# Kernel optimization log

Hardware: AMD Instinct MI355X
Metric: run time of the kernel (lower is better)

Reference implementation:

```python
import jax, jax.numpy as jnp
import numpy as np

STATE_DIM = 2
HIDDEN = 1024
N_SKILLS = 5
N_ACTIONS = 4
BATCH = 65536


def setup_inputs() -> dict:
    key = jax.random.key(0)
    ks = jax.random.split(key, 8)
    def lin_init(k, fan_in, shape):
        bound = 1.0 / np.sqrt(fan_in)
        return jax.random.uniform(k, shape, jnp.float32, -bound, bound)
    return {
        "s": jax.random.normal(ks[0], (BATCH, STATE_DIM), jnp.float32),
        "skill_idx": jax.random.randint(ks[1], (BATCH,), 0, N_SKILLS, jnp.int32),
        "W1": lin_init(ks[2], STATE_DIM, (STATE_DIM, HIDDEN)),
        "b1": lin_init(ks[3], STATE_DIM, (HIDDEN,)),
        "W2": lin_init(ks[4], HIDDEN, (HIDDEN, HIDDEN)),
        "b2": lin_init(ks[5], HIDDEN, (HIDDEN,)),
        "W_heads": lin_init(ks[6], HIDDEN, (N_SKILLS, HIDDEN, N_ACTIONS)),
        "b_heads": lin_init(ks[7], HIDDEN, (N_SKILLS, N_ACTIONS)),
    }


def reference(s, skill_idx, W1, b1, W2, b2, W_heads, b_heads):
    # shared feature MLP: Linear -> ReLU -> Linear -> ReLU
    h = jax.nn.relu(s @ W1 + b1)            # [B, H]
    feat = jax.nn.relu(h @ W2 + b2)         # [B, H]
    # per-sample skill head: gather weights then one batched contraction
    Wg = W_heads[skill_idx]                 # [B, H, A]
    bg = b_heads[skill_idx]                 # [B, A]
    return jnp.einsum('bh,bha->ba', feat, Wg) + bg  # [B, A]
```

## Files before the change

### kernel.cpp

```cpp
#include <hip/hip_runtime.h>

typedef __bf16 bf16x8 __attribute__((ext_vector_type(8)));
typedef __bf16 bf16x4 __attribute__((ext_vector_type(4)));
typedef float  floatx4 __attribute__((ext_vector_type(4)));

#define GLOBAL_AS __attribute__((address_space(1)))
#define LOCAL_AS  __attribute__((address_space(3)))

static constexpr int HID = 1024;
static constexpr int BM  = 256;
static constexpr int BN  = 256;
static constexpr int BK  = 32;
static constexpr int NT  = HID / BK;

__device__ __forceinline__ void h8(bf16x8& d, float s0, float s1,
                                   const float4& w0a, const float4& w0b,
                                   const float4& w1a, const float4& w1b,
                                   const float4& ba,  const float4& bb) {
    d[0] = (__bf16)fmaxf(fmaf(s1, w1a.x, fmaf(s0, w0a.x, ba.x)), 0.f);
    d[1] = (__bf16)fmaxf(fmaf(s1, w1a.y, fmaf(s0, w0a.y, ba.y)), 0.f);
    d[2] = (__bf16)fmaxf(fmaf(s1, w1a.z, fmaf(s0, w0a.z, ba.z)), 0.f);
    d[3] = (__bf16)fmaxf(fmaf(s1, w1a.w, fmaf(s0, w0a.w, ba.w)), 0.f);
    d[4] = (__bf16)fmaxf(fmaf(s1, w1b.x, fmaf(s0, w0b.x, bb.x)), 0.f);
    d[5] = (__bf16)fmaxf(fmaf(s1, w1b.y, fmaf(s0, w0b.y, bb.y)), 0.f);
    d[6] = (__bf16)fmaxf(fmaf(s1, w1b.z, fmaf(s0, w0b.z, bb.z)), 0.f);
    d[7] = (__bf16)fmaxf(fmaf(s1, w1b.w, fmaf(s0, w0b.w, bb.w)), 0.f);
}

__global__ __launch_bounds__(256)
void prep_all(const float* __restrict__ W2, const float* __restrict__ WH,
              __bf16* __restrict__ W2T, __bf16* __restrict__ WHT,
              float* __restrict__ OUT) {
    int b = blockIdx.x;
    if (b < 256) {
        ((float4*)OUT)[(size_t)b * 256 + threadIdx.x]
            = make_float4(0.f, 0.f, 0.f, 0.f);
        return;
    }
    b -= 256;
    if (b < 256) {
        __shared__ __align__(16) __bf16 tile[64][72];
        const int bx = b & 15;
        const int by = b >> 4;
        const int a  = threadIdx.x & 63;
        const int bb = threadIdx.x >> 6;
#pragma unroll
        for (int r = 0; r < 16; ++r) {
            const int k = r * 4 + bb;
            tile[a][k] = (__bf16)W2[(size_t)(by * 64 + k) * HID + bx * 64 + a];
        }
        __syncthreads();
        const int n_loc = threadIdx.x & 63;
        const int w     = threadIdx.x >> 6;
        const int nt    = bx >> 2;
        const int row   = (bx & 3) * 64 + n_loc;
#pragma unroll
        for (int h = 0; h < 2; ++h) {
            const int ko   = w * 2 + h;
            const int kt   = by * 2 + (ko >> 2);
            const int quad = ko & 3;
            const bf16x8 v = *(const bf16x8*)&tile[n_loc][ko * 8];
            const size_t idx = ((size_t)(nt * NT + kt) * 4 + quad) * 256 + row;
            *(bf16x8*)(W2T + idx * 8) = v;
        }
    } else {
        const int r = b - 256;
        const int s = r >> 2, a = r & 3;
        for (int k = threadIdx.x; k < HID; k += 256) {
            const float v = (r < 20) ? WH[((size_t)s * HID + k) * 4 + a] : 0.f;
            WHT[(size_t)(k >> 3) * 256 + r * 8 + (k & 7)] = (__bf16)v;
        }
    }
}

__global__ __launch_bounds__(512, 2)
void policy_main(const float* __restrict__ S,  const int* __restrict__ SK,
                 const float* __restrict__ W1, const float* __restrict__ B1,
                 const __bf16* __restrict__ W2T, const float* __restrict__ B2,
                 const __bf16* __restrict__ WHT, const float* __restrict__ BH,
                 float* __restrict__ OUT) {
    __shared__ __align__(16) char smem[131072];
    __bf16* A0    = (__bf16*)smem;
    __bf16* A1    = (__bf16*)(smem + 16384);
    __bf16* Bb    = (__bf16*)(smem + 32768);
    __bf16* featW = (__bf16*)smem;

    const int tid  = threadIdx.x;
    const int lane = tid & 63;
    const int wv   = tid >> 6;
    const int l15  = lane & 15;
    const int quad = lane >> 4;
    const int wm   = wv >> 2;
    const int wn   = wv & 3;
    const int n8   = blockIdx.x >> 8;
    const int g    = blockIdx.x & 255;
    const size_t i0 = (size_t)g * BM;

    const int octA = wv & 3;
    const int sgrp = wv >> 2;

    floatx4 acc[8][4] = {};

    float2 sv[2];
    sv[0] = *(const float2*)(S + (i0 + sgrp * 64 + lane) * 2);
    sv[1] = *(const float2*)(S + (i0 + 128 + sgrp * 64 + lane) * 2);

    float4 w0a = *(const float4*)(W1 + octA * 8);
    float4 w0b = *(const float4*)(W1 + octA * 8 + 4);
    float4 w1a = *(const float4*)(W1 + HID + octA * 8);
    float4 w1b = *(const float4*)(W1 + HID + octA * 8 + 4);
    float4 bba = *(const float4*)(B1 + octA * 8);
    float4 bbb = *(const float4*)(B1 + octA * 8 + 4);

#pragma unroll
    for (int t = 0; t < 2; ++t)
#pragma unroll
        for (int L = 0; L < 2; ++L) {
            const int c  = wv * 2 + L;
            const int q  = c >> 2;
            const int r0 = (c & 3) * 64;
            const __bf16* gp = W2T
                + ((size_t)((n8 * NT + t) * 4 + q) * 256 + r0 + lane) * 8;
            __builtin_amdgcn_global_load_lds((GLOBAL_AS void*)gp,
                (LOCAL_AS void*)(Bb + t * 8192 + (q * 256 + r0) * 8), 16, 0, 0);
        }

#pragma unroll
    for (int k = 0; k < 2; ++k) {
        const int smp = k * 128 + sgrp * 64 + lane;
        bf16x8 hv;
        h8(hv, sv[k].x, sv[k].y, w0a, w0b, w1a, w1b, bba, bbb);
        *(bf16x8*)(A0 + (octA * 256 + smp) * 8) = hv;
    }
    asm volatile("s_waitcnt vmcnt(2)" ::: "memory");
    asm volatile("s_waitcnt lgkmcnt(0)" ::: "memory");
    __builtin_amdgcn_s_barrier();

    int bcur = 0, bstg = 2;
#pragma unroll 1
    for (int t = 0; t < NT; ++t) {
        __bf16* Ac = (t & 1) ? A1 : A0;
        __bf16* An = (t & 1) ? A0 : A1;
        const __bf16* Bc = Bb + bcur * 8192;

        bf16x8 wf[4], hf[4];
#pragma unroll
        for (int f = 0; f < 4; ++f)
            wf[f] = *(const bf16x8*)(Bc + (quad * 256 + wn * 64 + f * 16 + l15) * 8);
#pragma unroll
        for (int f = 0; f < 4; ++f)
            hf[f] = *(const bf16x8*)(Ac + (quad * 256 + wm * 128 + f * 16 + l15) * 8);
        if (t < NT - 1) {
            const float* wp = W1 + (t + 1) * BK + octA * 8;
            w0a = *(const float4*)(wp);
            w0b = *(const float4*)(wp + 4);
            w1a = *(const float4*)(wp + HID);
            w1b = *(const float4*)(wp + HID + 4);
            bba = *(const float4*)(B1 + (t + 1) * BK + octA * 8);
            bbb = *(const float4*)(B1 + (t + 1) * BK + octA * 8 + 4);
        }
        if (t < NT - 2) {
#pragma unroll
            for (int L = 0; L < 2; ++L) {
                const int c  = wv * 2 + L;
                const int q  = c >> 2;
                const int r0 = (c & 3) * 64;
                const __bf16* gp = W2T
                    + ((size_t)((n8 * NT + (t + 2)) * 4 + q) * 256 + r0 + lane) * 8;
                __builtin_amdgcn_global_load_lds((GLOBAL_AS void*)gp,
                    (LOCAL_AS void*)(Bb + bstg * 8192 + (q * 256 + r0) * 8), 16, 0, 0);
            }
        }
        __builtin_amdgcn_s_barrier();
        asm volatile("s_waitcnt lgkmcnt(0)" ::: "memory");
        __builtin_amdgcn_s_setprio(1);
#pragma unroll
        for (int fm = 0; fm < 4; ++fm)
#pragma unroll
            for (int fn = 0; fn < 4; ++fn)
                acc[fm][fn] = __builtin_amdgcn_mfma_f32_16x16x32_bf16(
                    wf[fn], hf[fm], acc[fm][fn], 0, 0, 0);
        __builtin_amdgcn_s_setprio(0);
        __builtin_amdgcn_s_barrier();

        bf16x8 hf2[4];
#pragma unroll
        for (int f = 0; f < 4; ++f)
            hf2[f] = *(const bf16x8*)(Ac + (quad * 256 + wm * 128 + 64 + f * 16 + l15) * 8);
        if (t < NT - 1) {
#pragma unroll
            for (int k = 0; k < 2; ++k) {
                const int smp = k * 128 + sgrp * 64 + lane;
                bf16x8 hv;
                h8(hv, sv[k].x, sv[k].y, w0a, w0b, w1a, w1b, bba, bbb);
                *(bf16x8*)(An + (octA * 256 + smp) * 8) = hv;
            }
        }
        __builtin_amdgcn_s_barrier();
        asm volatile("s_waitcnt lgkmcnt(0)" ::: "memory");
        __builtin_amdgcn_s_setprio(1);
#pragma unroll
        for (int fm = 0; fm < 4; ++fm)
#pragma unroll
            for (int fn = 0; fn < 4; ++fn)
                acc[fm + 4][fn] = __builtin_amdgcn_mfma_f32_16x16x32_bf16(
                    wf[fn], hf2[fm], acc[fm + 4][fn], 0, 0, 0);
        __builtin_amdgcn_s_setprio(0);
        asm volatile("s_waitcnt vmcnt(2)" ::: "memory");
        __builtin_amdgcn_s_barrier();

        bcur = (bcur == 2) ? 0 : bcur + 1;
        bstg = (bstg == 2) ? 0 : bstg + 1;
    }

#pragma unroll
    for (int fn = 0; fn < 4; ++fn) {
        const int fcb = wn * 64 + fn * 16 + quad * 4;
        const float4 b2v = *(const float4*)(B2 + n8 * 256 + fcb);
        const int o = fcb >> 3, j = fcb & 7;
#pragma unroll
        for (int fm = 0; fm < 8; ++fm) {
            const int smp = wm * 128 + fm * 16 + l15;
            const floatx4 v = acc[fm][fn];
            bf16x4 p;
            p[0] = (__bf16)fmaxf(v[0] + b2v.x, 0.f);
            p[1] = (__bf16)fmaxf(v[1] + b2v.y, 0.f);
            p[2] = (__bf16)fmaxf(v[2] + b2v.z, 0.f);
            p[3] = (__bf16)fmaxf(v[3] + b2v.w, 0.f);
            *(bf16x4*)(featW + (o * 256 + smp) * 8 + j) = p;
        }
    }
    __syncthreads();

    floatx4 hacc[2][2] = {};
#pragma unroll
    for (int f2 = 0; f2 < 2; ++f2) {
        const int row = wv * 32 + f2 * 16 + l15;
#pragma unroll
        for (int ks2 = 0; ks2 < 8; ++ks2) {
            const bf16x8 fa = *(const bf16x8*)(featW
                                 + ((ks2 * 4 + quad) * 256 + row) * 8);
#pragma unroll
            for (int t2 = 0; t2 < 2; ++t2) {
                const int r  = t2 * 16 + l15;
                const int og = n8 * 32 + ks2 * 4 + quad;
                const bf16x8 wb = *(const bf16x8*)(WHT + ((size_t)og * 32 + r) * 8);
                hacc[f2][t2] = __builtin_amdgcn_mfma_f32_16x16x32_bf16(
                    fa, wb, hacc[f2][t2], 0, 0, 0);
            }
        }
    }

#pragma unroll
    for (int f2 = 0; f2 < 2; ++f2)
#pragma unroll
        for (int j = 0; j < 4; ++j) {
            const int smp = wv * 32 + f2 * 16 + quad * 4 + j;
            const int sk  = SK[i0 + smp];
#pragma unroll
            for (int t2 = 0; t2 < 2; ++t2) {
                const int hc = t2 * 16 + l15;
                const int d  = hc - sk * 4;
                if (d >= 0 && d < 4) {
                    float v = hacc[f2][t2][j];
                    if (n8 == 0) v += BH[hc];
                    atomicAdd(&OUT[(i0 + smp) * 4 + d], v);
                }
            }
        }
}

extern "C" void kernel_launch(void* const* d_in, const int* in_sizes, int n_in,
                              void* d_out, int out_size, void* d_ws, size_t ws_size,
                              hipStream_t stream) {
    const float* S  = (const float*)d_in[0];
    const int*   SK = (const int*)d_in[1];
    const float* W1 = (const float*)d_in[2];
    const float* B1 = (const float*)d_in[3];
    const float* W2 = (const float*)d_in[4];
    const float* B2 = (const float*)d_in[5];
    const float* WH = (const float*)d_in[6];
    const float* BH = (const float*)d_in[7];

    char* ws = (char*)d_ws;
    __bf16* W2T = (__bf16*)ws;
    __bf16* WHT = (__bf16*)(ws + 2 * 1024 * 1024);

    hipLaunchKernelGGL(prep_all, dim3(544), dim3(256), 0, stream,
                       W2, WH, W2T, WHT, (float*)d_out);
    hipLaunchKernelGGL(policy_main, dim3(1024), dim3(512), 0, stream,
                       S, SK, W1, B1, W2T, B2, WHT, BH, (float*)d_out);
}
```

Measured before the change: 263.2 us.

## Shrink LDS footprint and prefetch layer-1 weights two tiles ahead

Cuts shared memory per block from 128KB to 80KB by writing the second-layer features to LDS in two 128-column halves, running the head contraction on each half in turn. Moves the on-the-fly layer-1 activation generation for the next tile ahead of the first MFMA phase and prefetches the W1/B1 slices two tiles ahead, relaxing the vmcnt waits accordingly. The smaller LDS use may let more blocks reside per CU and hide the W1 load latency, at the cost of an extra barrier pass in the epilogue and more in-flight vector loads.

Measured after the change: 259.5 us. No clear change (-1.4%).

```diff
diff --git a/kernel.cpp b/kernel.cpp
--- a/kernel.cpp
+++ b/kernel.cpp
@@ -8,8 +8,6 @@
 #define LOCAL_AS  __attribute__((address_space(3)))
 
 static constexpr int HID = 1024;
-static constexpr int BM  = 256;
-static constexpr int BN  = 256;
 static constexpr int BK  = 32;
 static constexpr int NT  = HID / BK;
 
@@ -79,7 +77,7 @@
                  const __bf16* __restrict__ W2T, const float* __restrict__ B2,
                  const __bf16* __restrict__ WHT, const float* __restrict__ BH,
                  float* __restrict__ OUT) {
-    __shared__ __align__(16) char smem[131072];
+    __shared__ __align__(16) char smem[81920];
     __bf16* A0    = (__bf16*)smem;
     __bf16* A1    = (__bf16*)(smem + 16384);
     __bf16* Bb    = (__bf16*)(smem + 32768);
@@ -94,23 +92,26 @@
     const int wn   = wv & 3;
     const int n8   = blockIdx.x >> 8;
     const int g    = blockIdx.x & 255;
-    const size_t i0 = (size_t)g * BM;
+    const size_t i0 = (size_t)g * 256;
 
     const int octA = wv & 3;
     const int sgrp = wv >> 2;
 
     floatx4 acc[8][4] = {};
 
-    float2 sv[2];
-    sv[0] = *(const float2*)(S + (i0 + sgrp * 64 + lane) * 2);
-    sv[1] = *(const float2*)(S + (i0 + 128 + sgrp * 64 + lane) * 2);
-
-    float4 w0a = *(const float4*)(W1 + octA * 8);
-    float4 w0b = *(const float4*)(W1 + octA * 8 + 4);
-    float4 w1a = *(const float4*)(W1 + HID + octA * 8);
-    float4 w1b = *(const float4*)(W1 + HID + octA * 8 + 4);
-    float4 bba = *(const float4*)(B1 + octA * 8);
-    float4 bbb = *(const float4*)(B1 + octA * 8 + 4);
+    const float2 sv0 = *(const float2*)(S + (i0 + sgrp * 64 + lane) * 2);
+    const float2 sv1 = *(const float2*)(S + (i0 + 128 + sgrp * 64 + lane) * 2);
+
+    float4 w0a, w0b, w1a, w1b, bba, bbb;
+    {
+        const float* wp = W1 + octA * 8;
+        w0a = *(const float4*)(wp);
+        w0b = *(const float4*)(wp + 4);
+        w1a = *(const float4*)(wp + HID);
+        w1b = *(const float4*)(wp + HID + 4);
+        bba = *(const float4*)(B1 + octA * 8);
+        bbb = *(const float4*)(B1 + octA * 8 + 4);
+    }
 
 #pragma unroll
     for (int t = 0; t < 2; ++t)
@@ -125,15 +126,25 @@
                 (LOCAL_AS void*)(Bb + t * 8192 + (q * 256 + r0) * 8), 16, 0, 0);
         }
 
-#pragma unroll
-    for (int k = 0; k < 2; ++k) {
-        const int smp = k * 128 + sgrp * 64 + lane;
+    {
         bf16x8 hv;
-        h8(hv, sv[k].x, sv[k].y, w0a, w0b, w1a, w1b, bba, bbb);
-        *(bf16x8*)(A0 + (octA * 256 + smp) * 8) = hv;
-    }
-    asm volatile("s_waitcnt vmcnt(2)" ::: "memory");
-    asm volatile("s_waitcnt lgkmcnt(0)" ::: "memory");
+        h8(hv, sv0.x, sv0.y, w0a, w0b, w1a, w1b, bba, bbb);
+        *(bf16x8*)(A0 + (octA * 256 + sgrp * 64 + lane) * 8) = hv;
+        h8(hv, sv1.x, sv1.y, w0a, w0b, w1a, w1b, bba, bbb);
+        *(bf16x8*)(A0 + (octA * 256 + 128 + sgrp * 64 + lane) * 8) = hv;
+    }
+
+    {
+        const float* wp = W1 + BK + octA * 8;
+        w0a = *(const float4*)(wp);
+        w0b = *(const float4*)(wp + 4);
+        w1a = *(const float4*)(wp + HID);
+        w1b = *(const float4*)(wp + HID + 4);
+        bba = *(const float4*)(B1 + BK + octA * 8);
+        bbb = *(const float4*)(B1 + BK + octA * 8 + 4);
+    }
+
+    asm volatile("s_waitcnt vmcnt(8) lgkmcnt(0)" ::: "memory");
     __builtin_amdgcn_s_barrier();
 
     int bcur = 0, bstg = 2;
@@ -151,13 +162,20 @@
         for (int f = 0; f < 4; ++f)
             hf[f] = *(const bf16x8*)(Ac + (quad * 256 + wm * 128 + f * 16 + l15) * 8);
         if (t < NT - 1) {
-            const float* wp = W1 + (t + 1) * BK + octA * 8;
+            bf16x8 hv;
+            h8(hv, sv0.x, sv0.y, w0a, w0b, w1a, w1b, bba, bbb);
+            *(bf16x8*)(An + (octA * 256 + sgrp * 64 + lane) * 8) = hv;
+            h8(hv, sv1.x, sv1.y, w0a, w0b, w1a, w1b, bba, bbb);
+            *(bf16x8*)(An + (octA * 256 + 128 + sgrp * 64 + lane) * 8) = hv;
+        }
+        if (t < NT - 2) {
+            const float* wp = W1 + (t + 2) * BK + octA * 8;
             w0a = *(const float4*)(wp);
             w0b = *(const float4*)(wp + 4);
             w1a = *(const float4*)(wp + HID);
             w1b = *(const float4*)(wp + HID + 4);
-            bba = *(const float4*)(B1 + (t + 1) * BK + octA * 8);
-            bbb = *(const float4*)(B1 + (t + 1) * BK + octA * 8 + 4);
+            bba = *(const float4*)(B1 + (t + 2) * BK + octA * 8);
+            bbb = *(const float4*)(B1 + (t + 2) * BK + octA * 8 + 4);
         }
         if (t < NT - 2) {
 #pragma unroll
@@ -187,15 +205,6 @@
 #pragma unroll
         for (int f = 0; f < 4; ++f)
             hf2[f] = *(const bf16x8*)(Ac + (quad * 256 + wm * 128 + 64 + f * 16 + l15) * 8);
-        if (t < NT - 1) {
-#pragma unroll
-            for (int k = 0; k < 2; ++k) {
-                const int smp = k * 128 + sgrp * 64 + lane;
-                bf16x8 hv;
-                h8(hv, sv[k].x, sv[k].y, w0a, w0b, w1a, w1b, bba, bbb);
-                *(bf16x8*)(An + (octA * 256 + smp) * 8) = hv;
-            }
-        }
         __builtin_amdgcn_s_barrier();
         asm volatile("s_waitcnt lgkmcnt(0)" ::: "memory");
         __builtin_amdgcn_s_setprio(1);
@@ -206,49 +215,57 @@
                 acc[fm + 4][fn] = __builtin_amdgcn_mfma_f32_16x16x32_bf16(
                     wf[fn], hf2[fm], acc[fm + 4][fn], 0, 0, 0);
         __builtin_amdgcn_s_setprio(0);
-        asm volatile("s_waitcnt vmcnt(2)" ::: "memory");
+        if (t < NT - 2)
+            asm volatile("s_waitcnt vmcnt(8)" ::: "memory");
+        else
+            asm volatile("s_waitcnt vmcnt(0)" ::: "memory");
         __builtin_amdgcn_s_barrier();
 
         bcur = (bcur == 2) ? 0 : bcur + 1;
         bstg = (bstg == 2) ? 0 : bstg + 1;
     }
 
-#pragma unroll
-    for (int fn = 0; fn < 4; ++fn) {
-        const int fcb = wn * 64 + fn * 16 + quad * 4;
-        const float4 b2v = *(const float4*)(B2 + n8 * 256 + fcb);
-        const int o = fcb >> 3, j = fcb & 7;
-#pragma unroll
-        for (int fm = 0; fm < 8; ++fm) {
-            const int smp = wm * 128 + fm * 16 + l15;
-            const floatx4 v = acc[fm][fn];
-            bf16x4 p;
-            p[0] = (__bf16)fmaxf(v[0] + b2v.x, 0.f);
-            p[1] = (__bf16)fmaxf(v[1] + b2v.y, 0.f);
-            p[2] = (__bf16)fmaxf(v[2] + b2v.z, 0.f);
-            p[3] = (__bf16)fmaxf(v[3] + b2v.w, 0.f);
-            *(bf16x4*)(featW + (o * 256 + smp) * 8 + j) = p;
-        }
-    }
-    __syncthreads();
-
     floatx4 hacc[2][2] = {};
 #pragma unroll
-    for (int f2 = 0; f2 < 2; ++f2) {
-        const int row = wv * 32 + f2 * 16 + l15;
-#pragma unroll
-        for (int ks2 = 0; ks2 < 8; ++ks2) {
-            const bf16x8 fa = *(const bf16x8*)(featW
-                                 + ((ks2 * 4 + quad) * 256 + row) * 8);
-#pragma unroll
-            for (int t2 = 0; t2 < 2; ++t2) {
-                const int r  = t2 * 16 + l15;
-                const int og = n8 * 32 + ks2 * 4 + quad;
-                const bf16x8 wb = *(const bf16x8*)(WHT + ((size_t)og * 32 + r) * 8);
-                hacc[f2][t2] = __builtin_amdgcn_mfma_f32_16x16x32_bf16(
-                    fa, wb, hacc[f2][t2], 0, 0, 0);
+    for (int c = 0; c < 2; ++c) {
+        if ((wn >> 1) == c) {
+#pragma unroll
+            for (int fn = 0; fn < 4; ++fn) {
+                const int fcb = (wn & 1) * 64 + fn * 16 + quad * 4;
+                const float4 b2v = *(const float4*)(B2 + n8 * 256 + c * 128 + fcb);
+                const int o = fcb >> 3, j = fcb & 7;
+#pragma unroll
+                for (int fm = 0; fm < 8; ++fm) {
+                    const int smp = wm * 128 + fm * 16 + l15;
+                    const floatx4 v = acc[fm][fn];
+                    bf16x4 p;
+                    p[0] = (__bf16)fmaxf(v[0] + b2v.x, 0.f);
+                    p[1] = (__bf16)fmaxf(v[1] + b2v.y, 0.f);
+                    p[2] = (__bf16)fmaxf(v[2] + b2v.z, 0.f);
+                    p[3] = (__bf16)fmaxf(v[3] + b2v.w, 0.f);
+                    *(bf16x4*)(featW + (o * 256 + smp) * 8 + j) = p;
+                }
             }
         }
+        __syncthreads();
+#pragma unroll
+        for (int f2 = 0; f2 < 2; ++f2) {
+            const int row = wv * 32 + f2 * 16 + l15;
+#pragma unroll
+            for (int ks2 = 0; ks2 < 4; ++ks2) {
+                const bf16x8 fa = *(const bf16x8*)(featW
+                                     + ((ks2 * 4 + quad) * 256 + row) * 8);
+#pragma unroll
+                for (int t2 = 0; t2 < 2; ++t2) {
+                    const int r  = t2 * 16 + l15;
+                    const int og = n8 * 32 + c * 16 + ks2 * 4 + quad;
+                    const bf16x8 wb = *(const bf16x8*)(WHT + (size_t)og * 256 + r * 8);
+                    hacc[f2][t2] = __builtin_amdgcn_mfma_f32_16x16x32_bf16(
+                        fa, wb, hacc[f2][t2], 0, 0, 0);
+                }
+            }
+        }
+        __syncthreads();
     }
 
 #pragma unroll
```
